# Kernel tuning notes

Measured on AMD Instinct MI355X. Metric: run time of the kernel, lower is better.

Reference implementation:

```python
import jax, jax.numpy as jnp
import numpy as np

BN_EPS = 1e-6


def _conv1x1(x, w, b):
    # x: (B, Cin, N, K), w: (Cout, Cin), b: (Cout,)
    return jnp.einsum('oc,bcnk->bonk', w, x) + b[None, :, None, None]


def _bn(x, gamma, beta, mean, var):
    # inference-mode BatchNorm2d over channel axis 1
    inv = gamma / jnp.sqrt(var + BN_EPS)
    return x * inv[None, :, None, None] + (beta - mean * inv)[None, :, None, None]


def setup_inputs() -> dict:
    key = jax.random.key(0)
    ks = jax.random.split(key, 12)
    B, N, K = 4, 16384, 16
    C_out = 32
    C_img = 2 * C_out - 10          # 54, so concat has 2*C_out = 64 channels
    C_in1 = 2 * C_out               # 64
    C_in2 = 2 * (C_out + 3)         # 70

    points = jax.random.normal(ks[0], (B, N, 3), jnp.float32)
    image_features = jax.random.normal(ks[1], (B, C_img, N, K), jnp.float32)
    dist = jax.random.uniform(ks[2], (B, N, K), jnp.float32)
    idx = jax.random.randint(ks[3], (B, N, K), 0, N, dtype=jnp.int32)

    w1 = jax.random.normal(ks[4], (C_out, C_in1), jnp.float32) / np.sqrt(C_in1).astype(np.float32)
    b1 = jnp.zeros((C_out,), jnp.float32)
    gamma1 = jnp.ones((C_out,), jnp.float32)
    beta1 = jnp.zeros((C_out,), jnp.float32)
    mean1 = 0.1 * jax.random.normal(ks[5], (C_out,), jnp.float32)
    var1 = 0.5 + jax.random.uniform(ks[6], (C_out,), jnp.float32)

    w2 = jax.random.normal(ks[7], (C_out, C_in2), jnp.float32) / np.sqrt(C_in2).astype(np.float32)
    b2 = jnp.zeros((C_out,), jnp.float32)
    gamma2 = jnp.ones((C_out,), jnp.float32)
    beta2 = jnp.zeros((C_out,), jnp.float32)
    mean2 = 0.1 * jax.random.normal(ks[8], (C_out,), jnp.float32)
    var2 = 0.5 + jax.random.uniform(ks[9], (C_out,), jnp.float32)

    return {
        'points': points, 'image_features': image_features, 'dist': dist, 'idx': idx,
        'w1': w1, 'b1': b1, 'gamma1': gamma1, 'beta1': beta1, 'mean1': mean1, 'var1': var1,
        'w2': w2, 'b2': b2, 'gamma2': gamma2, 'beta2': beta2, 'mean2': mean2, 'var2': var2,
    }


def reference(points, image_features, dist, idx,
              w1, b1, gamma1, beta1, mean1, var1,
              w2, b2, gamma2, beta2, mean2, var2):
    B, N, K = idx.shape
    pts = jnp.swapaxes(points, 1, 2)                       # (B, 3, N)
    ep = jnp.broadcast_to(pts[:, :, :, None], (B, 3, N, K))  # extended points
    # KNN gather: nb[b, c, n, k] = pts[b, c, idx[b, n, k]]
    nb = jax.vmap(lambda p, i: p[:, i])(pts, idx)          # (B, 3, N, K)

    concat = jnp.concatenate(
        [ep, nb, ep - nb, dist[:, None, :, :], image_features], axis=1)  # (B, 64, N, K)

    h = jax.nn.relu(_bn(_conv1x1(concat, w1, b1), gamma1, beta1, mean1, var1))  # (B, 32, N, K)
    feat = jnp.concatenate([h, ep], axis=1)                # (B, 35, N, K)

    pooled = jnp.concatenate(
        [jnp.max(feat, axis=-1, keepdims=True),
         jnp.mean(feat, axis=-1, keepdims=True)], axis=1)  # (B, 70, N, 1)

    out = jax.nn.relu(_bn(_conv1x1(pooled, w2, b2), gamma2, beta2, mean2, var2))  # (B, 32, N, 1)
    return out
```

## Files before the change

### kernel.cpp

```cpp
#include <hip/hip_runtime.h>
#include <cmath>

#define BN_EPS 1e-6f
constexpr int B_     = 4;
constexpr int N_     = 16384;
constexpr int K_     = 16;
constexpr int C_IMG  = 54;
constexpr int C1     = 64;
constexpr int CO     = 32;
constexpr int C2     = 70;
constexpr int NT     = 16;
constexpr int HPAD   = 17;
constexpr int PPAD   = 76;
constexpr int NK     = N_ * K_;
constexpr int CHUNK  = 6;

__global__ __launch_bounds__(256, 4) void pif_fused_kernel(
    const float* __restrict__ points,
    const float* __restrict__ imgf,
    const float* __restrict__ dist,
    const int*   __restrict__ idx,
    const float* __restrict__ w1,
    const float* __restrict__ b1,
    const float* __restrict__ g1,
    const float* __restrict__ be1,
    const float* __restrict__ m1,
    const float* __restrict__ v1,
    const float* __restrict__ w2,
    const float* __restrict__ b2,
    const float* __restrict__ g2,
    const float* __restrict__ be2,
    const float* __restrict__ m2,
    const float* __restrict__ v2,
    float* __restrict__ out)
{
    __shared__ float h_lds[CO][NT * HPAD];
    __shared__ float pooled[NT][PPAD];

    const int t    = threadIdx.x;
    const int tpb  = N_ / NT;
    const int b    = blockIdx.x / tpb;
    const int n0   = (blockIdx.x % tpb) * NT;

    const int k    = t & 15;
    const int ln   = t >> 4;
    const int n    = n0 + ln;

    const int   base_nk = (b * N_ + n) * K_ + k;
    const int   j  = idx[base_nk];
    const float dv = dist[base_nk];

    const int pbase = (b * N_ + n) * 3;
    const float px = points[pbase + 0];
    const float py = points[pbase + 1];
    const float pz = points[pbase + 2];
    const int qb = (b * N_ + j) * 3;
    const float qx = points[qb + 0];
    const float qy = points[qb + 1];
    const float qz = points[qb + 2];

    float g[10];
    g[0] = px;      g[1] = py;      g[2] = pz;
    g[3] = qx;      g[4] = qy;      g[5] = qz;
    g[6] = px - qx; g[7] = py - qy; g[8] = pz - qz;
    g[9] = dv;

    float acc[CO];
    #pragma unroll
    for (int o = 0; o < CO; ++o) {
        const float* wr = w1 + o * C1;
        float a0 = 0.f, a1 = 0.f;
        #pragma unroll
        for (int c = 0; c < 10; c += 2) {
            a0 = fmaf(wr[c],     g[c],     a0);
            a1 = fmaf(wr[c + 1], g[c + 1], a1);
        }
        acc[o] = a0 + a1;
    }

    const float* ip = imgf + (size_t)b * C_IMG * NK + (n * K_ + k);
    #pragma unroll
    for (int c0 = 0; c0 < C_IMG; c0 += CHUNK) {
        float xv[CHUNK];
        #pragma unroll
        for (int jj = 0; jj < CHUNK; ++jj)
            xv[jj] = ip[(c0 + jj) * NK];
        #pragma unroll
        for (int o = 0; o < CO; ++o) {
            const float* wr = w1 + o * C1 + 10 + c0;
            #pragma unroll
            for (int jj = 0; jj < CHUNK; ++jj)
                acc[o] = fmaf(wr[jj], xv[jj], acc[o]);
        }
    }

    #pragma unroll
    for (int o = 0; o < CO; ++o) {
        const float inv = g1[o] * rsqrtf(v1[o] + BN_EPS);
        float hv = fmaf(acc[o] + b1[o], inv, be1[o] - m1[o] * inv);
        hv = fmaxf(hv, 0.f);
        h_lds[o][ln * HPAD + k] = hv;
    }
    __syncthreads();

    #pragma unroll
    for (int r = 0; r < 2; ++r) {
        const int nn = t & 15;
        const int c  = (t >> 4) + r * 16;
        float mx = 0.f;
        float sm = 0.f;
        #pragma unroll
        for (int kk = 0; kk < K_; ++kk) {
            const float v = h_lds[c][nn * HPAD + kk];
            mx = fmaxf(mx, v);
            sm += v;
        }
        pooled[nn][c]      = mx;
        pooled[nn][35 + c] = sm * (1.f / 16.f);
    }
    if (t < 48) {
        const int nn = t & 15;
        const int jj = t >> 4;
        const float v = points[(b * N_ + n0 + nn) * 3 + jj];
        pooled[nn][32 + jj] = v;
        pooled[nn][67 + jj] = v;
    }
    __syncthreads();

    #pragma unroll
    for (int r = 0; r < 2; ++r) {
        const int nn = t & 15;
        const int o  = (t >> 4) + r * 16;
        const float* wr = w2 + o * C2;
        float a0 = 0.f, a1 = 0.f;
        #pragma unroll
        for (int c = 0; c < C2; c += 2) {
            a0 = fmaf(wr[c],     pooled[nn][c],     a0);
            a1 = fmaf(wr[c + 1], pooled[nn][c + 1], a1);
        }
        const float acc2 = a0 + a1;
        const float inv = g2[o] * rsqrtf(v2[o] + BN_EPS);
        float ov = fmaf(acc2 + b2[o], inv, be2[o] - m2[o] * inv);
        ov = fmaxf(ov, 0.f);
        out[(b * CO + o) * N_ + n0 + nn] = ov;
    }
}

extern "C" void kernel_launch(void* const* d_in, const int* in_sizes, int n_in,
                              void* d_out, int out_size, void* d_ws, size_t ws_size,
                              hipStream_t stream) {
    const float* points = (const float*)d_in[0];
    const float* imgf   = (const float*)d_in[1];
    const float* dist   = (const float*)d_in[2];
    const int*   idx    = (const int*)  d_in[3];
    const float* w1     = (const float*)d_in[4];
    const float* b1     = (const float*)d_in[5];
    const float* g1     = (const float*)d_in[6];
    const float* be1    = (const float*)d_in[7];
    const float* m1     = (const float*)d_in[8];
    const float* v1     = (const float*)d_in[9];
    const float* w2     = (const float*)d_in[10];
    const float* b2     = (const float*)d_in[11];
    const float* g2     = (const float*)d_in[12];
    const float* be2    = (const float*)d_in[13];
    const float* m2     = (const float*)d_in[14];
    const float* v2     = (const float*)d_in[15];
    float* out          = (float*)d_out;

    const int blocks = B_ * (N_ / NT);
    pif_fused_kernel<<<blocks, 256, 0, stream>>>(
        points, imgf, dist, idx,
        w1, b1, g1, be1, m1, v1,
        w2, b2, g2, be2, m2, v2, out);
}
```

Measured before the change: 400.4 us.

## Compute first 1x1 conv with bf16 MFMA and pool via cross-lane shuffles

Each thread packs its 64 input channels (geometry plus image features) into bf16 pairs in LDS. Each wavefront then runs 16x16x32 bf16 MFMA instructions against weights held in registers, replacing the per-thread scalar FMA loop over 32 outputs by 64 inputs. The max and mean pooling over K are done directly on the accumulator registers with xor shuffles, which removes the intermediate h tile in LDS. Converting to bf16 lowers precision compared with the fp32 reference. The kernel is likely bound by reading image features from memory, so the compute savings may matter less than they appear.

```diff
diff --git a/kernel.cpp b/kernel.cpp
--- a/kernel.cpp
+++ b/kernel.cpp
@@ -1,129 +1,150 @@
 #include <hip/hip_runtime.h>
+#include <hip/hip_bf16.h>
 #include <cmath>
 
 #define BN_EPS 1e-6f
-constexpr int B_     = 4;
-constexpr int N_     = 16384;
-constexpr int K_     = 16;
-constexpr int C_IMG  = 54;
-constexpr int C1     = 64;
-constexpr int CO     = 32;
-constexpr int C2     = 70;
-constexpr int NT     = 16;
-constexpr int HPAD   = 17;
-constexpr int PPAD   = 76;
-constexpr int NK     = N_ * K_;
-constexpr int CHUNK  = 6;
+typedef unsigned int u32;
+typedef __attribute__((ext_vector_type(8))) short short8;
+typedef __attribute__((ext_vector_type(4))) float f32x4;
 
-__global__ __launch_bounds__(256, 4) void pif_fused_kernel(
-    const float* __restrict__ points,
-    const float* __restrict__ imgf,
-    const float* __restrict__ dist,
-    const int*   __restrict__ idx,
-    const float* __restrict__ w1,
-    const float* __restrict__ b1,
-    const float* __restrict__ g1,
-    const float* __restrict__ be1,
-    const float* __restrict__ m1,
-    const float* __restrict__ v1,
-    const float* __restrict__ w2,
-    const float* __restrict__ b2,
-    const float* __restrict__ g2,
-    const float* __restrict__ be2,
-    const float* __restrict__ m2,
-    const float* __restrict__ v2,
+constexpr int B_    = 4;
+constexpr int N_    = 16384;
+constexpr int K_    = 16;
+constexpr int C_IMG = 54;
+constexpr int C1    = 64;
+constexpr int CO    = 32;
+constexpr int C2    = 70;
+constexpr int NT    = 16;
+constexpr int POS   = 256;
+constexpr int XSTR  = 34;
+constexpr int PPAD  = 76;
+constexpr int NK    = N_ * K_;
+constexpr int CHUNK = 6;
+
+__device__ inline u32 pkbf(float a, float b) {
+    union { __hip_bfloat162 h; u32 u; } cv;
+    cv.h = __float22bfloat162_rn(make_float2(a, b));
+    return cv.u;
+}
+
+__global__ __launch_bounds__(256, 4) void pif_mfma_kernel(
+    const float* __restrict__ points, const float* __restrict__ imgf,
+    const float* __restrict__ dist,   const int*   __restrict__ idx,
+    const float* __restrict__ w1, const float* __restrict__ b1,
+    const float* __restrict__ g1, const float* __restrict__ be1,
+    const float* __restrict__ m1, const float* __restrict__ v1,
+    const float* __restrict__ w2, const float* __restrict__ b2,
+    const float* __restrict__ g2, const float* __restrict__ be2,
+    const float* __restrict__ m2, const float* __restrict__ v2,
     float* __restrict__ out)
 {
-    __shared__ float h_lds[CO][NT * HPAD];
+    __shared__ u32   x_lds[POS * XSTR];
     __shared__ float pooled[NT][PPAD];
 
-    const int t    = threadIdx.x;
-    const int tpb  = N_ / NT;
-    const int b    = blockIdx.x / tpb;
-    const int n0   = (blockIdx.x % tpb) * NT;
-
-    const int k    = t & 15;
-    const int ln   = t >> 4;
-    const int n    = n0 + ln;
+    const int t   = threadIdx.x;
+    const int tpb = N_ / NT;
+    const int b   = blockIdx.x / tpb;
+    const int n0  = (blockIdx.x % tpb) * NT;
+    const int k   = t & 15, ln = t >> 4, n = n0 + ln;
 
     const int   base_nk = (b * N_ + n) * K_ + k;
     const int   j  = idx[base_nk];
     const float dv = dist[base_nk];
+    const int   pb = (b * N_ + n) * 3;
+    const float px = points[pb], py = points[pb + 1], pz = points[pb + 2];
+    const int   qb = (b * N_ + j) * 3;
+    const float qx = points[qb], qy = points[qb + 1], qz = points[qb + 2];
 
-    const int pbase = (b * N_ + n) * 3;
-    const float px = points[pbase + 0];
-    const float py = points[pbase + 1];
-    const float pz = points[pbase + 2];
-    const int qb = (b * N_ + j) * 3;
-    const float qx = points[qb + 0];
-    const float qy = points[qb + 1];
-    const float qz = points[qb + 2];
-
-    float g[10];
-    g[0] = px;      g[1] = py;      g[2] = pz;
-    g[3] = qx;      g[4] = qy;      g[5] = qz;
-    g[6] = px - qx; g[7] = py - qy; g[8] = pz - qz;
-    g[9] = dv;
-
-    float acc[CO];
-    #pragma unroll
-    for (int o = 0; o < CO; ++o) {
-        const float* wr = w1 + o * C1;
-        float a0 = 0.f, a1 = 0.f;
-        #pragma unroll
-        for (int c = 0; c < 10; c += 2) {
-            a0 = fmaf(wr[c],     g[c],     a0);
-            a1 = fmaf(wr[c + 1], g[c + 1], a1);
-        }
-        acc[o] = a0 + a1;
-    }
+    u32* row = &x_lds[t * XSTR];
+    row[0] = pkbf(px, py);
+    row[1] = pkbf(pz, qx);
+    row[2] = pkbf(qy, qz);
+    row[3] = pkbf(px - qx, py - qy);
+    row[4] = pkbf(pz - qz, dv);
 
     const float* ip = imgf + (size_t)b * C_IMG * NK + (n * K_ + k);
     #pragma unroll
     for (int c0 = 0; c0 < C_IMG; c0 += CHUNK) {
         float xv[CHUNK];
         #pragma unroll
-        for (int jj = 0; jj < CHUNK; ++jj)
-            xv[jj] = ip[(c0 + jj) * NK];
+        for (int jj = 0; jj < CHUNK; ++jj) xv[jj] = ip[(c0 + jj) * NK];
+        row[5 + c0 / 2    ] = pkbf(xv[0], xv[1]);
+        row[5 + c0 / 2 + 1] = pkbf(xv[2], xv[3]);
+        row[5 + c0 / 2 + 2] = pkbf(xv[4], xv[5]);
+    }
+
+    const int w = t >> 6, lane = t & 63, m16 = lane & 15, quad = lane >> 4;
+
+    short8 bfrag[2][2];
+    float  inv1v[2], add1v[2];
+    #pragma unroll
+    for (int ot = 0; ot < 2; ++ot) {
+        const int o = ot * 16 + m16;
         #pragma unroll
-        for (int o = 0; o < CO; ++o) {
-            const float* wr = w1 + o * C1 + 10 + c0;
-            #pragma unroll
-            for (int jj = 0; jj < CHUNK; ++jj)
-                acc[o] = fmaf(wr[jj], xv[jj], acc[o]);
+        for (int kc = 0; kc < 2; ++kc) {
+            const float* wr = w1 + o * C1 + kc * 32 + quad * 8;
+            union { u32 u[4]; short8 v; } bf;
+            bf.u[0] = pkbf(wr[0], wr[1]); bf.u[1] = pkbf(wr[2], wr[3]);
+            bf.u[2] = pkbf(wr[4], wr[5]); bf.u[3] = pkbf(wr[6], wr[7]);
+            bfrag[ot][kc] = bf.v;
+        }
+        const float iv = g1[o] * rsqrtf(v1[o] + BN_EPS);
+        inv1v[ot] = iv;
+        add1v[ot] = be1[o] - m1[o] * iv + b1[o] * iv;
+    }
+
+    if (t < 48) {
+        const int nn = t & 15, jj = t >> 4;
+        const float v = points[(b * N_ + n0 + nn) * 3 + jj];
+        pooled[nn][32 + jj] = v;
+        pooled[nn][67 + jj] = v;
+    }
+
+    __syncthreads();
+
+    f32x4 acc[4][2];
+    #pragma unroll
+    for (int mt = 0; mt < 4; ++mt)
+        #pragma unroll
+        for (int ot = 0; ot < 2; ++ot)
+            acc[mt][ot] = (f32x4){0.f, 0.f, 0.f, 0.f};
+
+    #pragma unroll
+    for (int mt = 0; mt < 4; ++mt) {
+        #pragma unroll
+        for (int kc = 0; kc < 2; ++kc) {
+            const u32* r2 = &x_lds[(w * 64 + mt * 16 + m16) * XSTR + kc * 16 + quad * 4];
+            uint2 a0 = *(const uint2*)r2;
+            uint2 a1 = *(const uint2*)(r2 + 2);
+            union { u32 u[4]; short8 v; } af;
+            af.u[0] = a0.x; af.u[1] = a0.y; af.u[2] = a1.x; af.u[3] = a1.y;
+            acc[mt][0] = __builtin_amdgcn_mfma_f32_16x16x32_bf16(af.v, bfrag[0][kc], acc[mt][0], 0, 0, 0);
+            acc[mt][1] = __builtin_amdgcn_mfma_f32_16x16x32_bf16(af.v, bfrag[1][kc], acc[mt][1], 0, 0, 0);
         }
     }
 
     #pragma unroll
-    for (int o = 0; o < CO; ++o) {
-        const float inv = g1[o] * rsqrtf(v1[o] + BN_EPS);
-        float hv = fmaf(acc[o] + b1[o], inv, be1[o] - m1[o] * inv);
-        hv = fmaxf(hv, 0.f);
-        h_lds[o][ln * HPAD + k] = hv;
-    }
-    __syncthreads();
-
-    #pragma unroll
-    for (int r = 0; r < 2; ++r) {
-        const int nn = t & 15;
-        const int c  = (t >> 4) + r * 16;
-        float mx = 0.f;
-        float sm = 0.f;
+    for (int mt = 0; mt < 4; ++mt) {
         #pragma unroll
-        for (int kk = 0; kk < K_; ++kk) {
-            const float v = h_lds[c][nn * HPAD + kk];
-            mx = fmaxf(mx, v);
-            sm += v;
+        for (int ot = 0; ot < 2; ++ot) {
+            float mx = 0.f, sm = 0.f;
+            #pragma unroll
+            for (int r = 0; r < 4; ++r) {
+                float hv = fmaf(acc[mt][ot][r], inv1v[ot], add1v[ot]);
+                hv = fmaxf(hv, 0.f);
+                mx = fmaxf(mx, hv);
+                sm += hv;
+            }
+            mx = fmaxf(mx, __shfl_xor(mx, 16));
+            mx = fmaxf(mx, __shfl_xor(mx, 32));
+            sm += __shfl_xor(sm, 16);
+            sm += __shfl_xor(sm, 32);
+            if (quad == 0) {
+                const int nn = w * 4 + mt;
+                pooled[nn][ot * 16 + m16]      = mx;
+                pooled[nn][35 + ot * 16 + m16] = sm * (1.f / 16.f);
+            }
         }
-        pooled[nn][c]      = mx;
-        pooled[nn][35 + c] = sm * (1.f / 16.f);
-    }
-    if (t < 48) {
-        const int nn = t & 15;
-        const int jj = t >> 4;
-        const float v = points[(b * N_ + n0 + nn) * 3 + jj];
-        pooled[nn][32 + jj] = v;
-        pooled[nn][67 + jj] = v;
     }
     __syncthreads();
 
@@ -139,8 +160,8 @@
             a1 = fmaf(wr[c + 1], pooled[nn][c + 1], a1);
         }
         const float acc2 = a0 + a1;
-        const float inv = g2[o] * rsqrtf(v2[o] + BN_EPS);
-        float ov = fmaf(acc2 + b2[o], inv, be2[o] - m2[o] * inv);
+        const float iv = g2[o] * rsqrtf(v2[o] + BN_EPS);
+        float ov = fmaf(acc2 + b2[o], iv, be2[o] - m2[o] * iv);
         ov = fmaxf(ov, 0.f);
         out[(b * CO + o) * N_ + n0 + nn] = ov;
     }
@@ -168,7 +189,7 @@
     float* out          = (float*)d_out;
 
     const int blocks = B_ * (N_ / NT);
-    pif_fused_kernel<<<blocks, 256, 0, stream>>>(
+    pif_mfma_kernel<<<blocks, 256, 0, stream>>>(
         points, imgf, dist, idx,
         w1, b1, g1, be1, m1, v1,
         w2, b2, g2, be2, m2, v2, out);
```

Measured after the change: 356.3 us. 11.0% less time.
